# Kernel tuning notes

Measured on AMD Instinct MI355X. Metric: run time of the kernel, lower is better.

The kernel has to match this reference:

```python
import jax, jax.numpy as jnp
import numpy as np

N, IN_F, OUT_F = 10000, 512, 64
ALPHA = 0.2       # leaky relu slope
THRESHOLD = 0.01  # hub threshold
NEG_INF = -9.0e15


def setup_inputs() -> dict:
    key = jax.random.key(0)
    k_h, k_adj, k_hub, k_W, k_as, k_ad = jax.random.split(key, 6)
    h = jax.random.normal(k_h, (N, IN_F), dtype=jnp.float32)
    adj = jax.random.randint(k_adj, (N, N), 0, 2, dtype=jnp.int32)
    hub_mask = jax.random.uniform(k_hub, (N,), dtype=jnp.float32)
    # xavier-uniform-ish params (gain 1.414)
    lim_W = 1.414 * np.sqrt(6.0 / (IN_F + OUT_F))
    W = jax.random.uniform(k_W, (IN_F, OUT_F), minval=-lim_W, maxval=lim_W, dtype=jnp.float32)
    lim_a = 1.414 * np.sqrt(6.0 / (OUT_F + 1))
    a_src = jax.random.uniform(k_as, (OUT_F, 1), minval=-lim_a, maxval=lim_a, dtype=jnp.float32)
    a_dst = jax.random.uniform(k_ad, (OUT_F, 1), minval=-lim_a, maxval=lim_a, dtype=jnp.float32)
    return {"h": h, "W": W, "a_src": a_src, "a_dst": a_dst, "hub_mask": hub_mask, "adj": adj}


def reference(h, W, a_src, a_dst, hub_mask, adj):
    Wh = h @ W                                  # [N, F_out]
    e_src = Wh @ a_src                          # [N, 1]
    e_dst = Wh @ a_dst                          # [N, 1]
    e = jax.nn.leaky_relu(e_src + e_dst.T, negative_slope=ALPHA)  # [N, N]
    scores = jnp.where(adj > 0, e, jnp.float32(NEG_INF))
    attention = jax.nn.softmax(scores, axis=1)  # row-wise softmax over neighbors
    attention = jax.nn.relu(attention - hub_mask * THRESHOLD)  # hub threshold prune
    # dropout omitted (inference mode / p applied as no-op for deterministic reference)
    h_prime = attention @ Wh                    # [N, F_out]
    return jax.nn.elu(h_prime)                  # concat=True branch
```

## Files before the change

kernel.cpp:

```cpp
#include <hip/hip_runtime.h>
#include <math.h>

#define N_NODES 10000
#define IN_FEAT 512
#define OUT_FEAT 64
#define LRELU_ALPHA 0.2f
#define HUB_THRESH 0.01f
#define BITS_STRIDE 320

#define WH_OFF   0
#define ESRC_OFF 640000
#define EDST_OFF 650000
#define T_OFF    660000
#define LT_OFF   670000
#define L_OFF    680000
#define BITS_OFF 690000

__global__ __launch_bounds__(256) void k1_gemm(
    const float* __restrict__ h, const float* __restrict__ W,
    const float* __restrict__ a_src, const float* __restrict__ a_dst,
    const float* __restrict__ hub, float* __restrict__ ws)
{
    const int bx = blockIdx.x, tid = threadIdx.x;
    if (bx >= 625) {
        const int base = (bx - 625) * 1024;
        #pragma unroll
        for (int e = 0; e < 4; ++e) {
            int idx = base + e * 256 + tid;
            if (idx < N_NODES) {
                float t = hub[idx] * HUB_THRESH;
                ws[T_OFF + idx]  = t;
                ws[LT_OFF + idx] = logf(t);
            }
        }
        return;
    }

    __shared__ __align__(16) float Ws[64 * 64];
    __shared__ __align__(16) float Hs[16 * 64];
    const int col = tid & 63, rg = tid >> 6;
    const int rowBase = bx * 16;
    float acc[4] = {0.f, 0.f, 0.f, 0.f};

    for (int k0 = 0; k0 < IN_FEAT; k0 += 64) {
        for (int idx = tid; idx < 4096; idx += 256) {
            int kk = idx >> 6, c = idx & 63;
            Ws[idx] = W[(size_t)(k0 + kk) * 64 + c];
        }
        for (int idx = tid; idx < 1024; idx += 256) {
            int r = idx >> 6, kk = idx & 63;
            Hs[idx] = h[(size_t)(rowBase + r) * IN_FEAT + k0 + kk];
        }
        __syncthreads();
        #pragma unroll
        for (int k4 = 0; k4 < 16; ++k4) {
            float4 hv0 = *(const float4*)&Hs[(rg + 0)  * 64 + k4 * 4];
            float4 hv1 = *(const float4*)&Hs[(rg + 4)  * 64 + k4 * 4];
            float4 hv2 = *(const float4*)&Hs[(rg + 8)  * 64 + k4 * 4];
            float4 hv3 = *(const float4*)&Hs[(rg + 12) * 64 + k4 * 4];
            float w0 = Ws[(k4 * 4 + 0) * 64 + col];
            float w1 = Ws[(k4 * 4 + 1) * 64 + col];
            float w2 = Ws[(k4 * 4 + 2) * 64 + col];
            float w3 = Ws[(k4 * 4 + 3) * 64 + col];
            acc[0] += hv0.x * w0 + hv0.y * w1 + hv0.z * w2 + hv0.w * w3;
            acc[1] += hv1.x * w0 + hv1.y * w1 + hv1.z * w2 + hv1.w * w3;
            acc[2] += hv2.x * w0 + hv2.y * w1 + hv2.z * w2 + hv2.w * w3;
            acc[3] += hv3.x * w0 + hv3.y * w1 + hv3.z * w2 + hv3.w * w3;
        }
        __syncthreads();
    }

    const float asv = a_src[col], adv = a_dst[col];
    #pragma unroll
    for (int r = 0; r < 4; ++r) {
        int row = rowBase + rg + 4 * r;
        ws[WH_OFF + (size_t)row * 64 + col] = acc[r];
        float s1 = acc[r] * asv, s2 = acc[r] * adv;
        #pragma unroll
        for (int m = 32; m; m >>= 1) {
            s1 += __shfl_xor(s1, m, 64);
            s2 += __shfl_xor(s2, m, 64);
        }
        if (col == 0) {
            ws[ESRC_OFF + row] = s1;
            ws[EDST_OFF + row] = s2;
        }
    }
}

__global__ __launch_bounds__(256) void k2_stats(
    const int* __restrict__ adj, float* __restrict__ ws,
    unsigned* __restrict__ wsu)
{
    const int i = blockIdx.x, tid = threadIdx.x;
    const int lane = tid & 63;
    const float esrc = ws[ESRC_OFF + i];
    const float* __restrict__ edst = ws + EDST_OFF;
    const int4* __restrict__ arow = (const int4*)(adj + (size_t)i * N_NODES);
    unsigned* __restrict__ brow = wsu + BITS_OFF + (size_t)i * BITS_STRIDE;
    float acc = 0.f;

    #pragma unroll
    for (int it = 0; it < 10; ++it) {
        const int j0 = it * 1024 + tid * 4;
        unsigned nib = 0;
        if (j0 < N_NODES) {
            int4 a4  = arow[j0 >> 2];
            float4 e4 = *(const float4*)(edst + j0);
            float s, e;
            s = esrc + e4.x; e = fmaxf(s, LRELU_ALPHA * s);
            if (a4.x > 0) { acc += __expf(e); nib |= 1u; }
            s = esrc + e4.y; e = fmaxf(s, LRELU_ALPHA * s);
            if (a4.y > 0) { acc += __expf(e); nib |= 2u; }
            s = esrc + e4.z; e = fmaxf(s, LRELU_ALPHA * s);
            if (a4.z > 0) { acc += __expf(e); nib |= 4u; }
            s = esrc + e4.w; e = fmaxf(s, LRELU_ALPHA * s);
            if (a4.w > 0) { acc += __expf(e); nib |= 8u; }
        }
        unsigned v = nib << ((lane & 7) * 4);
        v |= (unsigned)__shfl_xor((int)v, 1, 64);
        v |= (unsigned)__shfl_xor((int)v, 2, 64);
        v |= (unsigned)__shfl_xor((int)v, 4, 64);
        if ((lane & 7) == 0) {
            int widx = j0 >> 5;
            if (widx < BITS_STRIDE) brow[widx] = v;
        }
    }

    #pragma unroll
    for (int m = 32; m; m >>= 1) acc += __shfl_xor(acc, m, 64);
    __shared__ float part[4];
    if (lane == 0) part[tid >> 6] = acc;
    __syncthreads();
    if (tid == 0) ws[L_OFF + i] = part[0] + part[1] + part[2] + part[3];
}

__global__ __launch_bounds__(256) void k3_aggr(
    const float* __restrict__ ws, const unsigned* __restrict__ wsu,
    float* __restrict__ out)
{
    const int i = blockIdx.x, tid = threadIdx.x;
    const int lane = tid & 63, w = tid >> 6;
    const float l = ws[L_OFF + i];
    const float esrc = ws[ESRC_OFF + i];
    const bool empty = (l == 0.0f);
    const float cl = empty ? 0.0f : logf(l);
    const float invN = 1.0f / (float)N_NODES;
    const float* __restrict__ edst  = ws + EDST_OFF;
    const float* __restrict__ tarr  = ws + T_OFF;
    const float* __restrict__ ltarr = ws + LT_OFF;
    const float* __restrict__ Wh    = ws + WH_OFF;
    const unsigned* __restrict__ brow = wsu + BITS_OFF + (size_t)i * BITS_STRIDE;
    float acc = 0.f;

    const int ngroups = (N_NODES + 63) >> 6;
    for (int g = w; g < ngroups; g += 4) {
        const int j = g * 64 + lane;
        const int jc = j < N_NODES ? j : N_NODES - 1;
        const unsigned word = brow[j >> 5];
        const bool bit = (word >> (j & 31)) & 1u;
        const float ed = edst[jc];
        const float s = esrc + ed;
        const float e = fmaxf(s, LRELU_ALPHA * s);
        float wgt = 0.0f;
        if (empty) {
            if (j < N_NODES) wgt = fmaxf(invN - tarr[jc], 0.0f);
        } else {
            bool cand = (j < N_NODES) && bit && (e > cl + ltarr[jc] - 0.0625f);
            if (cand) {
                float p = __expf(e - cl);
                wgt = fmaxf(p - tarr[jc], 0.0f);
            }
        }
        unsigned long long mk = __ballot(wgt > 0.0f);
        while (mk) {
            int src = __builtin_ctzll(mk);
            mk &= mk - 1;
            float wv = __shfl(wgt, src, 64);
            int jj = g * 64 + src;
            acc += wv * Wh[(size_t)jj * 64 + lane];
        }
    }

    __shared__ float part[256];
    part[tid] = acc;
    __syncthreads();
    if (w == 0) {
        float tot = part[lane] + part[64 + lane] + part[128 + lane] + part[192 + lane];
        out[(size_t)i * 64 + lane] = tot > 0.0f ? tot : expm1f(tot);
    }
}

extern "C" void kernel_launch(void* const* d_in, const int* in_sizes, int n_in,
                              void* d_out, int out_size, void* d_ws, size_t ws_size,
                              hipStream_t stream)
{
    const float* h     = (const float*)d_in[0];
    const float* W     = (const float*)d_in[1];
    const float* a_src = (const float*)d_in[2];
    const float* a_dst = (const float*)d_in[3];
    const float* hub   = (const float*)d_in[4];
    const int*   adj   = (const int*)d_in[5];
    float*    ws  = (float*)d_ws;
    unsigned* wsu = (unsigned*)d_ws;
    float*    out = (float*)d_out;

    k1_gemm<<<635, 256, 0, stream>>>(h, W, a_src, a_dst, hub, ws);
    k2_stats<<<N_NODES, 256, 0, stream>>>(adj, ws, wsu);
    k3_aggr<<<N_NODES, 256, 0, stream>>>(ws, wsu, out);
}
```

Measured before the change: 711.9 us.

## Fuse softmax-stats and aggregation kernels, keep adjacency bitmask in shared memory

Merges the row-statistics kernel and the aggregation kernel into one per-row kernel. The packed adjacency bitmask and the softmax denominator now stay in shared memory and registers, so they are no longer written to and read back from global workspace. This removes one kernel launch and a round trip of about 12.8 MB of bitmask data. In exchange each block does both phases in sequence, so its shared-memory use and lifetime grow, and overlap between the two phases across blocks may change.

Result: faster. 673.7 us (-5.4%).

```diff
diff --git a/kernel.cpp b/kernel.cpp
--- a/kernel.cpp
+++ b/kernel.cpp
@@ -6,15 +6,13 @@
 #define OUT_FEAT 64
 #define LRELU_ALPHA 0.2f
 #define HUB_THRESH 0.01f
-#define BITS_STRIDE 320
+#define BITS_WORDS 320
 
 #define WH_OFF   0
 #define ESRC_OFF 640000
 #define EDST_OFF 650000
 #define T_OFF    660000
 #define LT_OFF   670000
-#define L_OFF    680000
-#define BITS_OFF 690000
 
 __global__ __launch_bounds__(256) void k1_gemm(
     const float* __restrict__ h, const float* __restrict__ W,
@@ -88,16 +86,19 @@
     }
 }
 
-__global__ __launch_bounds__(256) void k2_stats(
-    const int* __restrict__ adj, float* __restrict__ ws,
-    unsigned* __restrict__ wsu)
+__global__ __launch_bounds__(256) void k2_fused(
+    const int* __restrict__ adj, const float* __restrict__ ws,
+    float* __restrict__ out)
 {
     const int i = blockIdx.x, tid = threadIdx.x;
-    const int lane = tid & 63;
+    const int lane = tid & 63, w = tid >> 6;
+    __shared__ unsigned bits[BITS_WORDS];
+    __shared__ float partA[4];
+    __shared__ float partB[256];
+
     const float esrc = ws[ESRC_OFF + i];
     const float* __restrict__ edst = ws + EDST_OFF;
     const int4* __restrict__ arow = (const int4*)(adj + (size_t)i * N_NODES);
-    unsigned* __restrict__ brow = wsu + BITS_OFF + (size_t)i * BITS_STRIDE;
     float acc = 0.f;
 
     #pragma unroll
@@ -121,43 +122,28 @@
         v |= (unsigned)__shfl_xor((int)v, 1, 64);
         v |= (unsigned)__shfl_xor((int)v, 2, 64);
         v |= (unsigned)__shfl_xor((int)v, 4, 64);
-        if ((lane & 7) == 0) {
-            int widx = j0 >> 5;
-            if (widx < BITS_STRIDE) brow[widx] = v;
-        }
+        if ((lane & 7) == 0) bits[j0 >> 5] = v;
     }
 
     #pragma unroll
     for (int m = 32; m; m >>= 1) acc += __shfl_xor(acc, m, 64);
-    __shared__ float part[4];
-    if (lane == 0) part[tid >> 6] = acc;
+    if (lane == 0) partA[w] = acc;
     __syncthreads();
-    if (tid == 0) ws[L_OFF + i] = part[0] + part[1] + part[2] + part[3];
-}
+    const float l = partA[0] + partA[1] + partA[2] + partA[3];
 
-__global__ __launch_bounds__(256) void k3_aggr(
-    const float* __restrict__ ws, const unsigned* __restrict__ wsu,
-    float* __restrict__ out)
-{
-    const int i = blockIdx.x, tid = threadIdx.x;
-    const int lane = tid & 63, w = tid >> 6;
-    const float l = ws[L_OFF + i];
-    const float esrc = ws[ESRC_OFF + i];
     const bool empty = (l == 0.0f);
     const float cl = empty ? 0.0f : logf(l);
     const float invN = 1.0f / (float)N_NODES;
-    const float* __restrict__ edst  = ws + EDST_OFF;
     const float* __restrict__ tarr  = ws + T_OFF;
     const float* __restrict__ ltarr = ws + LT_OFF;
     const float* __restrict__ Wh    = ws + WH_OFF;
-    const unsigned* __restrict__ brow = wsu + BITS_OFF + (size_t)i * BITS_STRIDE;
-    float acc = 0.f;
+    acc = 0.f;
 
     const int ngroups = (N_NODES + 63) >> 6;
     for (int g = w; g < ngroups; g += 4) {
         const int j = g * 64 + lane;
         const int jc = j < N_NODES ? j : N_NODES - 1;
-        const unsigned word = brow[j >> 5];
+        const unsigned word = bits[j >> 5];
         const bool bit = (word >> (j & 31)) & 1u;
         const float ed = edst[jc];
         const float s = esrc + ed;
@@ -182,11 +168,10 @@
         }
     }
 
-    __shared__ float part[256];
-    part[tid] = acc;
+    partB[tid] = acc;
     __syncthreads();
     if (w == 0) {
-        float tot = part[lane] + part[64 + lane] + part[128 + lane] + part[192 + lane];
+        float tot = partB[lane] + partB[64 + lane] + partB[128 + lane] + partB[192 + lane];
         out[(size_t)i * 64 + lane] = tot > 0.0f ? tot : expm1f(tot);
     }
 }
@@ -201,11 +186,9 @@
     const float* a_dst = (const float*)d_in[3];
     const float* hub   = (const float*)d_in[4];
     const int*   adj   = (const int*)d_in[5];
-    float*    ws  = (float*)d_ws;
-    unsigned* wsu = (unsigned*)d_ws;
-    float*    out = (float*)d_out;
+    float* ws  = (float*)d_ws;
+    float* out = (float*)d_out;
 
     k1_gemm<<<635, 256, 0, stream>>>(h, W, a_src, a_dst, hub, ws);
-    k2_stats<<<N_NODES, 256, 0, stream>>>(adj, ws, wsu);
-    k3_aggr<<<N_NODES, 256, 0, stream>>>(ws, wsu, out);
+    k2_fused<<<N_NODES, 256, 0, stream>>>(adj, ws, out);
 }
```
